# Optimization experiments

Measured on AMD Instinct MI355X. Metric: run time of the kernel, lower is better.

The kernel has to match this reference:

```python
import jax, jax.numpy as jnp
import numpy as np
import math

B_SZ, T_LEN, DIM = 1, 1024, 1024
D_STATE, EXPAND, NUM_SCALES, CONV_K = 16, 2, 3, 4
D_INNER = EXPAND * DIM
EPS_LOG = 1e-38
LN_EPS = 1e-5


def _causal_dwconv(x, w, b):
    # x: (B,T,D), w: (D,1,K) depthwise, b: (D,). torch Conv1d(pad=K-1)[:, :, :T] == left-pad K-1 (causal).
    y = jax.lax.conv_general_dilated(
        jnp.transpose(x, (0, 2, 1)), w, window_strides=(1,),
        padding=[(CONV_K - 1, 0)], dimension_numbers=('NCH', 'OIH', 'NCH'),
        feature_group_count=w.shape[0])
    return jnp.transpose(y, (0, 2, 1)) + b


def _ssm_core(x, cw, cb, xw, dtw, dtb, Dp):
    # x: (B,T,d_inner)
    xc = jax.nn.silu(_causal_dwconv(x, cw, cb))
    proj = xc @ xw.T                               # (B,T,2*d_state)
    B_ssm, C_ssm = proj[..., :D_STATE], proj[..., D_STATE:]
    dt = jax.nn.softplus(B_ssm @ dtw.T + dtb)      # (B,T,d_inner)
    dt = jax.nn.softplus(dt)                       # selective_scan applies softplus a second time (faithful)
    A = -jnp.arange(1, D_STATE + 1, dtype=xc.dtype)  # (d_state,) == -A_init row, same for every d_inner channel
    dA = jnp.exp(dt[..., None] * A)                # (B,T,d_inner,d_state)
    dBx = dt[..., None] * B_ssm[:, :, None, :] * xc[..., None]
    log_dA = jnp.log(jnp.clip(dA, EPS_LOG))
    log_dBx = jnp.log(jnp.clip(dBx, EPS_LOG))
    # parallel_scan_cpu: h = exp(cumsum(log_dA) + logcumsumexp(log_dBx - cumsum(log_dA)))
    a_star = jnp.cumsum(log_dA, axis=1)
    h = jnp.exp(a_star + jax.lax.cumlogsumexp(log_dBx - a_star, axis=1))
    return jnp.einsum('bts,btds->btd', C_ssm, h) + Dp * xc


def _downsample(x, stride):
    if stride == 1:
        return x
    Bb, T, D = x.shape
    Tt = (T // stride) * stride
    return x[:, :Tt].reshape(Bb, Tt // stride, stride, D).mean(2)


def _upsample(x, T_out):
    # F.interpolate(mode='linear', align_corners=False)
    T_in = x.shape[1]
    if T_in == T_out:
        return x
    scale = T_in / T_out
    pos = jnp.clip((jnp.arange(T_out, dtype=jnp.float32) + 0.5) * scale - 0.5, 0.0, T_in - 1)
    lo = jnp.floor(pos).astype(jnp.int32)
    hi = jnp.minimum(lo + 1, T_in - 1)
    w = (pos - lo.astype(pos.dtype))[None, :, None]
    return x[:, lo] * (1.0 - w) + x[:, hi] * w


def _forward(x, in_proj_w, conv_w, conv_b, xproj_w, dtproj_w, dtproj_b,
             D_param, scale_weights, gate_w1, gate_w2, out_proj_w, ln_g, ln_b):
    residual = x
    xz = x @ in_proj_w.T                           # (B,T,2*d_inner)
    x_in, gate = xz[..., :D_INNER], xz[..., D_INNER:]
    outs = []
    for s in range(NUM_SCALES):
        x_s = _downsample(x_in, 2 ** s)
        y_s = _ssm_core(x_s, conv_w[s], conv_b[s], xproj_w[s], dtproj_w[s], dtproj_b[s], D_param[s])
        outs.append(_upsample(y_s, x.shape[1]))
    w = jax.nn.softmax(scale_weights)
    fused = sum(w[s] * outs[s] for s in range(NUM_SCALES))
    ctx = sum(outs) / NUM_SCALES
    gate_ctx = jax.nn.sigmoid(jax.nn.silu(ctx @ gate_w1.T) @ gate_w2.T)
    out = (fused * gate_ctx) * jax.nn.silu(gate)
    out = out @ out_proj_w.T
    y = out + residual
    mu = y.mean(-1, keepdims=True)
    var = ((y - mu) ** 2).mean(-1, keepdims=True)
    return (y - mu) / jnp.sqrt(var + LN_EPS) * ln_g + ln_b


def setup_inputs() -> dict:
    key = jax.random.key(0)
    ks = jax.random.split(key, 12)
    g = lambda k, shp, s: (jax.random.normal(k, shp, jnp.float32) * s)
    return {
        'x': g(ks[0], (B_SZ, T_LEN, DIM), 1.0),
        'in_proj_w': g(ks[1], (2 * D_INNER, DIM), DIM ** -0.5),
        'conv_w': g(ks[2], (NUM_SCALES, D_INNER, 1, CONV_K), CONV_K ** -0.5),
        'conv_b': g(ks[3], (NUM_SCALES, D_INNER), 0.02),
        'xproj_w': g(ks[4], (NUM_SCALES, 2 * D_STATE, D_INNER), D_INNER ** -0.5),
        'dtproj_w': g(ks[5], (NUM_SCALES, D_INNER, D_STATE), D_STATE ** -0.5),
        'dtproj_b': jax.random.uniform(ks[6], (NUM_SCALES, D_INNER), jnp.float32,
                                       math.log(0.001), math.log(0.1)),
        'D_param': jnp.ones((NUM_SCALES, D_INNER), jnp.float32),
        'scale_weights': jnp.ones((NUM_SCALES,), jnp.float32) / NUM_SCALES,
        'gate_w1': g(ks[7], (D_INNER // 2, D_INNER), D_INNER ** -0.5),
        'gate_w2': g(ks[8], (D_INNER, D_INNER // 2), (D_INNER // 2) ** -0.5),
        'out_proj_w': g(ks[9], (DIM, D_INNER), D_INNER ** -0.5),
        'ln_g': jnp.ones((DIM,), jnp.float32),
        'ln_b': jnp.zeros((DIM,), jnp.float32),
    }


def reference(x, in_proj_w, conv_w, conv_b, xproj_w, dtproj_w, dtproj_b,
              D_param, scale_weights, gate_w1, gate_w2, out_proj_w, ln_g, ln_b):
    return _forward(x, in_proj_w, conv_w, conv_b, xproj_w, dtproj_w, dtproj_b,
                    D_param, scale_weights, gate_w1, gate_w2, out_proj_w, ln_g, ln_b)
```

## Files before the change

kernel.cpp:

```cpp
#include <hip/hip_runtime.h>

typedef unsigned short u16;
typedef float floatx4 __attribute__((ext_vector_type(4)));
typedef short shortx8 __attribute__((ext_vector_type(8)));

#define DIN 2048

__device__ __forceinline__ u16 f2bf(float f){
  unsigned u = __float_as_uint(f);
  u = (u + 0x7fffu + ((u>>16)&1u))>>16;
  return (u16)u;
}
__device__ __forceinline__ float sigf(float x){ return 1.f/(1.f+__expf(-x)); }
__device__ __forceinline__ float siluf(float x){ return x*sigf(x); }
__device__ __forceinline__ float softplusf(float x){ return fmaxf(x,0.f)+log1pf(__expf(-fabsf(x))); }

__device__ __forceinline__ void gld_lds16(const void* g, void* l){
  __builtin_amdgcn_global_load_lds((const __attribute__((address_space(1))) unsigned*)g,
                                   (__attribute__((address_space(3))) unsigned*)l, 16, 0, 0);
}

#define OFF_WINP  0ull
#define OFF_WG1   8388608ull
#define OFF_WG2   12582912ull
#define OFF_WOP   16777216ull
#define OFF_XB    20971520ull
#define OFF_XIN   23068672ull
#define OFF_SGATE 31457280ull
#define OFF_X1    39845888ull
#define OFF_X2    44040192ull
#define OFF_XC0   46137344ull
#define OFF_XC1   54525952ull
#define OFF_XC2   58720256ull
#define OFF_FUSED 60817408ull
#define OFF_G3O   69206016ull
#define OFF_Y0    75497472ull
#define OFF_Y1    83886080ull
#define OFF_Y2    88080384ull
#define OFF_P0    90177536ull
#define OFF_P1    90308608ull
#define OFF_P2    90374144ull
#define OFF_CTXB  OFF_XC0
#define OFF_T1B   OFF_XC1
#define OFF_PS    OFF_Y0
#define OFF_HINIT OFF_XIN
#define OFF_T1A0  OFF_XIN
#define OFF_T1A1  OFF_X1
#define OFF_YPA0  OFF_Y1
#define OFF_YPA1  (OFF_XC0 + 4194304ull)

__global__ __launch_bounds__(256) void cvt_kernel(
    const float* __restrict__ s0, u16* __restrict__ d0,
    const float* __restrict__ s1, u16* __restrict__ d1,
    const float* __restrict__ s2, u16* __restrict__ d2,
    const float* __restrict__ s3, u16* __restrict__ d3,
    const float* __restrict__ s4, u16* __restrict__ d4)
{
  int i = (blockIdx.x*256 + threadIdx.x)*4;
  const float* s; u16* d;
  if      (i <  4194304){ s=s0; d=d0; }
  else if (i <  6291456){ s=s1; d=d1; i -=  4194304; }
  else if (i <  8388608){ s=s2; d=d2; i -=  6291456; }
  else if (i < 10485760){ s=s3; d=d3; i -=  8388608; }
  else                  { s=s4; d=d4; i -= 10485760; }
  const float4 v = *(const float4*)(s + i);
  ushort4 o; o.x = f2bf(v.x); o.y = f2bf(v.y); o.z = f2bf(v.z); o.w = f2bf(v.w);
  *(ushort4*)(d + i) = o;
}

template<int MODE, int BM>
__global__ __launch_bounds__(256) void gemm_bt(
    const u16* __restrict__ A, const u16* __restrict__ B,
    int N, int K, int Ks,
    float* __restrict__ out_f, float* __restrict__ out_f2, u16* __restrict__ out_b,
    const float* __restrict__ ex0f, const float* __restrict__ ex1f,
    float* __restrict__ ex0, float* __restrict__ ex1)
{
  constexpr int NI = BM/32;
  constexpr int IP = BM/64;
  __shared__ u16 smA[2][BM*32];
  __shared__ u16 smB[2][BM*32];
  const int tid  = threadIdx.x;
  const int m0   = blockIdx.y * BM;
  const int n0   = blockIdx.x * BM;
  const int wv   = tid >> 6;
  const int lane = tid & 63;
  const int mw   = (wv >> 1) * (BM/2);
  const int nw   = (wv & 1) * (BM/2);
  const int quad = lane >> 4;
  const int l16  = lane & 15;
  const int srow = tid >> 2;
  const int scol = (tid & 3) * 8;

  floatx4 acc[NI][NI];
#pragma unroll
  for (int i=0;i<NI;i++)
#pragma unroll
    for (int j=0;j<NI;j++) acc[i][j] = (floatx4)0.f;

  const int kStart = blockIdx.z * Ks;
  const int kEnd   = kStart + Ks;

  auto stage = [&](int buf, int k0){
#pragma unroll
    for (int p=0;p<IP;p++){
      gld_lds16(A + (size_t)(m0 + p*64 + srow)*K + k0 + scol, &smA[buf][p*2048 + wv*512]);
      gld_lds16(B + (size_t)(n0 + p*64 + srow)*K + k0 + scol, &smB[buf][p*2048 + wv*512]);
    }
  };

  stage(0, kStart);
  int cur = 0;
  for (int k0 = kStart; k0 < kEnd; k0 += 32) {
    __syncthreads();
    if (k0 + 32 < kEnd) stage(cur^1, k0+32);
    shortx8 af[NI], bfr[NI];
#pragma unroll
    for (int i=0;i<NI;i++){
      af[i]  = *(const shortx8*)&smA[cur][(mw + i*16 + l16)*32 + quad*8];
      bfr[i] = *(const shortx8*)&smB[cur][(nw + i*16 + l16)*32 + quad*8];
    }
#pragma unroll
    for (int i=0;i<NI;i++)
#pragma unroll
      for (int j=0;j<NI;j++)
        acc[i][j] = __builtin_amdgcn_mfma_f32_16x16x32_bf16(af[i], bfr[j], acc[i][j], 0, 0, 0);
    cur ^= 1;
  }

#pragma unroll
  for (int i=0;i<NI;i++){
    const int mb = m0 + mw + i*16 + quad*4;
#pragma unroll
    for (int j=0;j<NI;j++){
      const int n = n0 + nw + j*16 + l16;
      const floatx4 v4 = acc[i][j];
      if (MODE == 0){
        if (n < 2048){
#pragma unroll
          for (int r=0;r<4;r++) out_f[(size_t)(mb+r)*2048 + n] = v4[r];
          ex0[(size_t)(mb>>1)*2048 + n]       = 0.5f*(v4[0]+v4[1]);
          ex0[(size_t)((mb>>1)+1)*2048 + n]   = 0.5f*(v4[2]+v4[3]);
          ex1[(size_t)(mb>>2)*2048 + n]       = 0.25f*(v4[0]+v4[1]+v4[2]+v4[3]);
        } else {
#pragma unroll
          for (int r=0;r<4;r++) out_f2[(size_t)(mb+r)*2048 + (n-2048)] = siluf(v4[r]);
        }
      } else if (MODE == 2){
#pragma unroll
        for (int r=0;r<4;r++){
          const size_t idx = (size_t)(mb+r)*N + n;
          out_b[idx] = f2bf(sigf(v4[r]) * ex0f[idx] * ex1f[idx]);
        }
      } else {
        float* dst = blockIdx.z ? out_f2 : out_f;
#pragma unroll
        for (int r=0;r<4;r++) dst[(size_t)(mb+r)*N + n] = v4[r];
      }
    }
  }
}

__global__ __launch_bounds__(256) void g2_epi(const float* __restrict__ a,
    const float* __restrict__ b, u16* __restrict__ o){
  const int i = (blockIdx.x*256 + threadIdx.x)*4;
  const float4 va = *(const float4*)(a+i);
  const float4 vb = *(const float4*)(b+i);
  ushort4 r;
  r.x = f2bf(siluf(va.x+vb.x)); r.y = f2bf(siluf(va.y+vb.y));
  r.z = f2bf(siluf(va.z+vb.z)); r.w = f2bf(siluf(va.w+vb.w));
  *(ushort4*)(o+i) = r;
}

__global__ __launch_bounds__(256) void conv_kernel(const float* __restrict__ xin,
    const float* __restrict__ x1, const float* __restrict__ x2,
    const float* __restrict__ cw, const float* __restrict__ cb,
    float* __restrict__ xc0, float* __restrict__ xc1, float* __restrict__ xc2){
  const int idx = blockIdx.x*256 + threadIdx.x;
  const float* xs; float* xc; int s, local;
  if (idx < 1024*DIN)              { s=0; local=idx;             xs=xin; xc=xc0; }
  else if (idx < (1024+512)*DIN)   { s=1; local=idx-1024*DIN;    xs=x1;  xc=xc1; }
  else                             { s=2; local=idx-1536*DIN;    xs=x2;  xc=xc2; }
  const int t = local >> 11, d = local & 2047;
  const float* w = cw + ((size_t)(s*DIN) + d)*4;
  float acc = cb[s*DIN + d];
#pragma unroll
  for (int j=0;j<4;j++){
    const int tt = t - 3 + j;
    if (tt >= 0) acc += w[j] * xs[(size_t)tt*DIN + d];
  }
  xc[local] = siluf(acc);
}

__global__ __launch_bounds__(256) void xproj_kernel(const float* __restrict__ xc0,
    const float* __restrict__ xc1, const float* __restrict__ xc2,
    const float* __restrict__ xw,
    float* __restrict__ p0, float* __restrict__ p1, float* __restrict__ p2){
  __shared__ float srow[DIN];
  const int b = blockIdx.x;
  const float* xc; float* proj; int s, t;
  if (b < 1024)      { s=0; t=b;       xc=xc0; proj=p0; }
  else if (b < 1536) { s=1; t=b-1024;  xc=xc1; proj=p1; }
  else               { s=2; t=b-1536;  xc=xc2; proj=p2; }
  const float* xr = xc + (size_t)t*DIN;
  const int tid = threadIdx.x;
#pragma unroll
  for (int q=0;q<2;q++){
    const int k = (q*256 + tid)*4;
    *(float4*)&srow[k] = *(const float4*)&xr[k];
  }
  __syncthreads();
  const int i = tid >> 3;
  const int j = tid & 7;
  const float* w = xw + ((size_t)s*32 + i)*DIN;
  float acc = 0.f;
#pragma unroll 8
  for (int c=0;c<256;c++){
    const int k = j + 8*c;
    acc += srow[k]*w[k];
  }
  acc += __shfl_xor(acc,1); acc += __shfl_xor(acc,2); acc += __shfl_xor(acc,4);
  if (j == 0) proj[t*32 + i] = acc;
}

__global__ __launch_bounds__(256) void scan_p1(
    const float* __restrict__ xc0, const float* __restrict__ xc1, const float* __restrict__ xc2,
    const float* __restrict__ p0,  const float* __restrict__ p1,  const float* __restrict__ p2,
    const float* __restrict__ dtw, const float* __restrict__ dtb,
    float2* __restrict__ PS)
{
  __shared__ float sproj[32*32];
  int b = blockIdx.x;
  const float *xc, *proj; int base, s;
  if (b < 256)      { xc=xc0; proj=p0; base=0;  s=0; }
  else if (b < 384) { b-=256; xc=xc1; proj=p1; base=32; s=1; }
  else              { b-=384; xc=xc2; proj=p2; base=48; s=2; }
  const int chunk = b >> 3;
  const int d     = (b & 7)*256 + threadIdx.x;
  const int t0    = chunk*32;
  {
    const int k = threadIdx.x*4;
    *(float4*)&sproj[k] = *(const float4*)&proj[t0*32 + k];
  }
  __syncthreads();

  float wreg[16];
  const float* wr = dtw + ((size_t)(s*DIN) + d)*16;
#pragma unroll
  for (int n=0;n<16;n++) wreg[n] = wr[n];
  const float bias = dtb[s*DIN + d];

  float H[16], P[16];
#pragma unroll
  for (int n=0;n<16;n++){ H[n]=0.f; P[n]=1.f; }
  const float* xcp = xc + (size_t)t0*DIN + d;
  float xcn = xcp[0];
  for (int tt=0; tt<32; tt++){
    const float xcv = xcn;
    if (tt < 31) xcn = xcp[(size_t)(tt+1)*DIN];
    const float* Bp = &sproj[tt*32];
    float bs = bias;
#pragma unroll
    for (int n=0;n<16;n++) bs += Bp[n]*wreg[n];
    const float dtv = softplusf(softplusf(bs));
    const float e = __expf(-dtv);
    const float c = dtv*xcv;
    float ep = e;
#pragma unroll
    for (int n=0;n<16;n++){
      const float dA  = fmaxf(ep, 1e-38f);
      const float dBx = fmaxf(c*Bp[n], 1e-38f);
      H[n] = dA*H[n] + dBx;
      P[n] *= dA;
      ep *= e;
    }
  }
  float2* o = PS + ((size_t)(base+chunk)*2048 + d)*16;
#pragma unroll
  for (int n=0;n<16;n++){ float2 v; v.x=P[n]; v.y=H[n]; o[n]=v; }
}

__global__ __launch_bounds__(256) void scan_combine(const float2* __restrict__ PS,
                                                    float* __restrict__ Hinit){
  int id = blockIdx.x*256 + threadIdx.x;
  int base, C;
  if (id < 32768)      { base=0;  C=32; }
  else if (id < 65536) { id-=32768; base=32; C=16; }
  else                 { id-=65536; base=48; C=8;  }
  const size_t off = (size_t)base*32768 + id;
  const float2* ps = PS + off;
  float* hi = Hinit + off;
  float H = 0.f;
  for (int c=0;c<C;c++){
    hi[(size_t)c*32768] = H;
    const float2 v = ps[(size_t)c*32768];
    H = v.x*H + v.y;
  }
}

__global__ __launch_bounds__(256) void scan_p2(
    const float* __restrict__ xc0, const float* __restrict__ xc1, const float* __restrict__ xc2,
    const float* __restrict__ p0,  const float* __restrict__ p1,  const float* __restrict__ p2,
    const float* __restrict__ dtw, const float* __restrict__ dtb,
    const float* __restrict__ Hinit, const float* __restrict__ Dp_all,
    float* __restrict__ y0, float* __restrict__ y1, float* __restrict__ y2)
{
  __shared__ float sproj[32*32];
  int b = blockIdx.x;
  const float *xc, *proj; float* y; int base, s;
  if (b < 256)      { xc=xc0; proj=p0; y=y0; base=0;  s=0; }
  else if (b < 384) { b-=256; xc=xc1; proj=p1; y=y1; base=32; s=1; }
  else              { b-=384; xc=xc2; proj=p2; y=y2; base=48; s=2; }
  const int chunk = b >> 3;
  const int d     = (b & 7)*256 + threadIdx.x;
  const int t0    = chunk*32;
  {
    const int k = threadIdx.x*4;
    *(float4*)&sproj[k] = *(const float4*)&proj[t0*32 + k];
  }
  __syncthreads();

  float wreg[16];
  const float* wr = dtw + ((size_t)(s*DIN) + d)*16;
#pragma unroll
  for (int n=0;n<16;n++) wreg[n] = wr[n];
  const float bias = dtb[s*DIN + d];

  float H[16];
  const float* hi = Hinit + ((size_t)(base+chunk)*2048 + d)*16;
#pragma unroll
  for (int n=0;n<16;n++) H[n] = hi[n];
  const float Dv = Dp_all[s*DIN + d];
  const float* xcp = xc + (size_t)t0*DIN + d;
  float* yp = y + (size_t)t0*DIN + d;
  float xcn = xcp[0];
  for (int tt=0; tt<32; tt++){
    const float xcv = xcn;
    if (tt < 31) xcn = xcp[(size_t)(tt+1)*DIN];
    const float* Bp = &sproj[tt*32];
    float bs = bias;
#pragma unroll
    for (int n=0;n<16;n++) bs += Bp[n]*wreg[n];
    const float dtv = softplusf(softplusf(bs));
    const float e = __expf(-dtv);
    const float c = dtv*xcv;
    float ep = e;
    float pacc = 0.f;
#pragma unroll
    for (int n=0;n<16;n++){
      const float dA  = fmaxf(ep, 1e-38f);
      const float dBx = fmaxf(c*Bp[n], 1e-38f);
      H[n] = dA*H[n] + dBx;
      pacc += Bp[16+n]*H[n];
      ep *= e;
    }
    yp[(size_t)tt*DIN] = pacc + Dv*xcv;
  }
}

__device__ __forceinline__ float ups_read(const float* __restrict__ ys, int Tin, int t, int d){
  const float scale = (float)Tin * (1.f/1024.f);
  float pos = ((float)t + 0.5f)*scale - 0.5f;
  pos = fminf(fmaxf(pos, 0.f), (float)(Tin-1));
  const int lo = (int)floorf(pos);
  const float w = pos - (float)lo;
  const int hi = min(lo+1, Tin-1);
  return ys[(size_t)lo*DIN + d]*(1.f-w) + ys[(size_t)hi*DIN + d]*w;
}

__global__ __launch_bounds__(256) void fuse_kernel(const float* __restrict__ y0,
    const float* __restrict__ y1, const float* __restrict__ y2,
    const float* __restrict__ sw, u16* __restrict__ ctxb, float* __restrict__ fused){
  const int idx = blockIdx.x*256 + threadIdx.x;
  const int t = idx >> 11, d = idx & 2047;
  const float w0r = sw[0], w1r = sw[1], w2r = sw[2];
  const float mx = fmaxf(w0r, fmaxf(w1r, w2r));
  float e0 = __expf(w0r-mx), e1 = __expf(w1r-mx), e2 = __expf(w2r-mx);
  const float inv = 1.f/(e0+e1+e2);
  e0 *= inv; e1 *= inv; e2 *= inv;
  const float o0 = y0[idx];
  const float o1 = ups_read(y1, 512, t, d);
  const float o2 = ups_read(y2, 256, t, d);
  fused[idx] = e0*o0 + e1*o1 + e2*o2;
  ctxb[idx]  = f2bf((o0+o1+o2)*(1.f/3.f));
}

__global__ __launch_bounds__(256) void ln_kernel(const float* __restrict__ ya,
    const float* __restrict__ yb, const float* __restrict__ xr,
    const float* __restrict__ g, const float* __restrict__ b, float* __restrict__ out){
  __shared__ float red[4];
  const int t = blockIdx.x;
  const size_t ro = (size_t)t*1024;
  float v[4];
  float s = 0.f;
#pragma unroll
  for (int i=0;i<4;i++){
    const int c = threadIdx.x + i*256;
    v[i] = ya[ro+c] + yb[ro+c] + xr[ro+c];
    s += v[i];
  }
  s += __shfl_xor(s,1); s += __shfl_xor(s,2); s += __shfl_xor(s,4);
  s += __shfl_xor(s,8); s += __shfl_xor(s,16); s += __shfl_xor(s,32);
  if ((threadIdx.x & 63) == 0) red[threadIdx.x>>6] = s;
  __syncthreads();
  const float mu = (red[0]+red[1]+red[2]+red[3]) * (1.f/1024.f);
  __syncthreads();
  float q = 0.f;
#pragma unroll
  for (int i=0;i<4;i++){ const float dd = v[i]-mu; q += dd*dd; }
  q += __shfl_xor(q,1); q += __shfl_xor(q,2); q += __shfl_xor(q,4);
  q += __shfl_xor(q,8); q += __shfl_xor(q,16); q += __shfl_xor(q,32);
  if ((threadIdx.x & 63) == 0) red[threadIdx.x>>6] = q;
  __syncthreads();
  const float rstd = rsqrtf((red[0]+red[1]+red[2]+red[3]) * (1.f/1024.f) + 1e-5f);
#pragma unroll
  for (int i=0;i<4;i++){
    const int c = threadIdx.x + i*256;
    out[ro + c] = (v[i]-mu)*rstd*g[c] + b[c];
  }
}

extern "C" void kernel_launch(void* const* d_in, const int* in_sizes, int n_in,
                              void* d_out, int out_size, void* d_ws, size_t ws_size,
                              hipStream_t stream) {
  const float* x     = (const float*)d_in[0];
  const float* inpw  = (const float*)d_in[1];
  const float* convw = (const float*)d_in[2];
  const float* convb = (const float*)d_in[3];
  const float* xpw   = (const float*)d_in[4];
  const float* dtw   = (const float*)d_in[5];
  const float* dtb   = (const float*)d_in[6];
  const float* Dp    = (const float*)d_in[7];
  const float* sw    = (const float*)d_in[8];
  const float* gw1   = (const float*)d_in[9];
  const float* gw2   = (const float*)d_in[10];
  const float* opw   = (const float*)d_in[11];
  const float* lng   = (const float*)d_in[12];
  const float* lnb   = (const float*)d_in[13];
  float* out = (float*)d_out;

  char* ws = (char*)d_ws;
  u16*    wInp  = (u16*)   (ws + OFF_WINP);
  u16*    wG1   = (u16*)   (ws + OFF_WG1);
  u16*    wG2   = (u16*)   (ws + OFF_WG2);
  u16*    wOp   = (u16*)   (ws + OFF_WOP);
  u16*    xb    = (u16*)   (ws + OFF_XB);
  float*  xin   = (float*) (ws + OFF_XIN);
  float*  sgate = (float*) (ws + OFF_SGATE);
  float*  x1    = (float*) (ws + OFF_X1);
  float*  x2    = (float*) (ws + OFF_X2);
  float*  xc0   = (float*) (ws + OFF_XC0);
  float*  xc1   = (float*) (ws + OFF_XC1);
  float*  xc2   = (float*) (ws + OFF_XC2);
  float*  y0    = (float*) (ws + OFF_Y0);
  float*  y1    = (float*) (ws + OFF_Y1);
  float*  y2    = (float*) (ws + OFF_Y2);
  float*  p0    = (float*) (ws + OFF_P0);
  float*  p1    = (float*) (ws + OFF_P1);
  float*  p2    = (float*) (ws + OFF_P2);
  float2* PS    = (float2*)(ws + OFF_PS);
  float*  Hinit = (float*) (ws + OFF_HINIT);
  u16*    ctxb  = (u16*)   (ws + OFF_CTXB);
  u16*    t1b   = (u16*)   (ws + OFF_T1B);
  float*  fused = (float*) (ws + OFF_FUSED);
  u16*    g3o   = (u16*)   (ws + OFF_G3O);
  float*  t1a0  = (float*) (ws + OFF_T1A0);
  float*  t1a1  = (float*) (ws + OFF_T1A1);
  float*  ypa0  = (float*) (ws + OFF_YPA0);
  float*  ypa1  = (float*) (ws + OFF_YPA1);

  cvt_kernel<<<11264, 256, 0, stream>>>(inpw, wInp, gw1, wG1, gw2, wG2, opw, wOp, x, xb);
  gemm_bt<0,64><<<dim3(64, 16, 1), 256, 0, stream>>>(xb, wInp, 4096, 1024, 1024,
                                                     xin, sgate, nullptr, nullptr, nullptr, x1, x2);
  conv_kernel<<<(1792*DIN)/256, 256, 0, stream>>>(xin, x1, x2, convw, convb, xc0, xc1, xc2);
  xproj_kernel<<<1792, 256, 0, stream>>>(xc0, xc1, xc2, xpw, p0, p1, p2);
  scan_p1<<<448, 256, 0, stream>>>(xc0, xc1, xc2, p0, p1, p2, dtw, dtb, PS);
  scan_combine<<<384, 256, 0, stream>>>(PS, Hinit);
  scan_p2<<<448, 256, 0, stream>>>(xc0, xc1, xc2, p0, p1, p2, dtw, dtb,
                                   Hinit, Dp, y0, y1, y2);
  fuse_kernel<<<(1024*DIN)/256, 256, 0, stream>>>(y0, y1, y2, sw, ctxb, fused);
  gemm_bt<4,64><<<dim3(16, 16, 2), 256, 0, stream>>>(ctxb, wG1, 1024, 2048, 1024,
                                                     t1a0, t1a1, nullptr, nullptr, nullptr, nullptr, nullptr);
  g2_epi<<<1024, 256, 0, stream>>>(t1a0, t1a1, t1b);
  gemm_bt<2,64><<<dim3(32, 16, 1), 256, 0, stream>>>(t1b, wG2, 2048, 1024, 1024,
                                                     nullptr, nullptr, g3o, fused, sgate, nullptr, nullptr);
  gemm_bt<4,64><<<dim3(16, 16, 2), 256, 0, stream>>>(g3o, wOp, 1024, 2048, 1024,
                                                     ypa0, ypa1, nullptr, nullptr, nullptr, nullptr, nullptr);
  ln_kernel<<<1024, 256, 0, stream>>>(ypa0, ypa1, x, lng, lnb, out);
}
```

Before: 343.8 us.

## Split scan state across thread pairs, cache dt, and use closed-form chunk decay

```diff
diff --git a/kernel.cpp b/kernel.cpp
--- a/kernel.cpp
+++ b/kernel.cpp
@@ -48,6 +48,9 @@
 #define OFF_T1A1  OFF_X1
 #define OFF_YPA0  OFF_Y1
 #define OFF_YPA1  (OFF_XC0 + 4194304ull)
+#define OFF_DT0   OFF_FUSED
+#define OFF_DT1   OFF_G3O
+#define OFF_DT2   (OFF_G3O + 4194304ull)
 
 __global__ __launch_bounds__(256) void cvt_kernel(
     const float* __restrict__ s0, u16* __restrict__ d0,
@@ -227,57 +230,64 @@
     const float* __restrict__ xc0, const float* __restrict__ xc1, const float* __restrict__ xc2,
     const float* __restrict__ p0,  const float* __restrict__ p1,  const float* __restrict__ p2,
     const float* __restrict__ dtw, const float* __restrict__ dtb,
+    float* __restrict__ dt0, float* __restrict__ dt1, float* __restrict__ dt2,
     float2* __restrict__ PS)
 {
   __shared__ float sproj[32*32];
   int b = blockIdx.x;
-  const float *xc, *proj; int base, s;
-  if (b < 256)      { xc=xc0; proj=p0; base=0;  s=0; }
-  else if (b < 384) { b-=256; xc=xc1; proj=p1; base=32; s=1; }
-  else              { b-=384; xc=xc2; proj=p2; base=48; s=2; }
-  const int chunk = b >> 3;
-  const int d     = (b & 7)*256 + threadIdx.x;
+  const float *xc, *proj; float* dto; int base, s;
+  if (b < 512)      { xc=xc0; proj=p0; dto=dt0; base=0;  s=0; }
+  else if (b < 768) { b-=512; xc=xc1; proj=p1; dto=dt1; base=32; s=1; }
+  else              { b-=768; xc=xc2; proj=p2; dto=dt2; base=48; s=2; }
+  const int chunk = b >> 4;
+  const int tid   = threadIdx.x;
+  const int d     = (b & 15)*128 + (tid >> 1);
+  const int half  = tid & 1;
+  const int n0    = half*8;
   const int t0    = chunk*32;
-  {
-    const int k = threadIdx.x*4;
-    *(float4*)&sproj[k] = *(const float4*)&proj[t0*32 + k];
-  }
-  __syncthreads();
-
-  float wreg[16];
-  const float* wr = dtw + ((size_t)(s*DIN) + d)*16;
-#pragma unroll
-  for (int n=0;n<16;n++) wreg[n] = wr[n];
+  { const int k = tid*4; *(float4*)&sproj[k] = *(const float4*)&proj[t0*32 + k]; }
+  __syncthreads();
+
+  float wreg[8];
+  const float* wr = dtw + ((size_t)(s*DIN) + d)*16 + n0;
+#pragma unroll
+  for (int k=0;k<8;k++) wreg[k] = wr[k];
   const float bias = dtb[s*DIN + d];
 
-  float H[16], P[16];
-#pragma unroll
-  for (int n=0;n<16;n++){ H[n]=0.f; P[n]=1.f; }
+  float H[8];
+#pragma unroll
+  for (int k=0;k<8;k++) H[k] = 0.f;
+  float S = 0.f;
   const float* xcp = xc + (size_t)t0*DIN + d;
-  float xcn = xcp[0];
+  float* dtp = dto + (size_t)t0*DIN + d;
   for (int tt=0; tt<32; tt++){
-    const float xcv = xcn;
-    if (tt < 31) xcn = xcp[(size_t)(tt+1)*DIN];
+    const float xcv = xcp[(size_t)tt*DIN];
     const float* Bp = &sproj[tt*32];
-    float bs = bias;
-#pragma unroll
-    for (int n=0;n<16;n++) bs += Bp[n]*wreg[n];
-    const float dtv = softplusf(softplusf(bs));
+    float bs = 0.f;
+#pragma unroll
+    for (int k=0;k<8;k++) bs += Bp[n0+k]*wreg[k];
+    bs += __shfl_xor(bs, 1);
+    const float dtv = softplusf(softplusf(bs + bias));
+    if (half == 0) dtp[(size_t)tt*DIN] = dtv;
+    S += dtv;
     const float e = __expf(-dtv);
+    const float e2 = e*e, e4 = e2*e2, e8 = e4*e4;
+    float ep = half ? e8*e : e;
     const float c = dtv*xcv;
-    float ep = e;
-#pragma unroll
-    for (int n=0;n<16;n++){
+#pragma unroll
+    for (int k=0;k<8;k++){
       const float dA  = fmaxf(ep, 1e-38f);
-      const float dBx = fmaxf(c*Bp[n], 1e-38f);
-      H[n] = dA*H[n] + dBx;
-      P[n] *= dA;
+      const float dBx = fmaxf(c*Bp[n0+k], 1e-38f);
+      H[k] = dA*H[k] + dBx;
       ep *= e;
     }
   }
-  float2* o = PS + ((size_t)(base+chunk)*2048 + d)*16;
-#pragma unroll
-  for (int n=0;n<16;n++){ float2 v; v.x=P[n]; v.y=H[n]; o[n]=v; }
+  const float q = __expf(-S);
+  const float q2 = q*q, q4 = q2*q2, q8 = q4*q4;
+  float qp = half ? q8*q : q;
+  float2* o = PS + ((size_t)(base+chunk)*2048 + d)*16 + n0;
+#pragma unroll
+  for (int k=0;k<8;k++){ float2 v; v.x = qp; v.y = H[k]; o[k] = v; qp *= q; }
 }
 
 __global__ __launch_bounds__(256) void scan_combine(const float2* __restrict__ PS,
@@ -301,60 +311,52 @@
 __global__ __launch_bounds__(256) void scan_p2(
     const float* __restrict__ xc0, const float* __restrict__ xc1, const float* __restrict__ xc2,
     const float* __restrict__ p0,  const float* __restrict__ p1,  const float* __restrict__ p2,
-    const float* __restrict__ dtw, const float* __restrict__ dtb,
+    const float* __restrict__ dt0, const float* __restrict__ dt1, const float* __restrict__ dt2,
     const float* __restrict__ Hinit, const float* __restrict__ Dp_all,
     float* __restrict__ y0, float* __restrict__ y1, float* __restrict__ y2)
 {
   __shared__ float sproj[32*32];
   int b = blockIdx.x;
-  const float *xc, *proj; float* y; int base, s;
-  if (b < 256)      { xc=xc0; proj=p0; y=y0; base=0;  s=0; }
-  else if (b < 384) { b-=256; xc=xc1; proj=p1; y=y1; base=32; s=1; }
-  else              { b-=384; xc=xc2; proj=p2; y=y2; base=48; s=2; }
-  const int chunk = b >> 3;
-  const int d     = (b & 7)*256 + threadIdx.x;
+  const float *xc, *proj, *dti; float* y; int base, s;
+  if (b < 512)      { xc=xc0; proj=p0; dti=dt0; y=y0; base=0;  s=0; }
+  else if (b < 768) { b-=512; xc=xc1; proj=p1; dti=dt1; y=y1; base=32; s=1; }
+  else              { b-=768; xc=xc2; proj=p2; dti=dt2; y=y2; base=48; s=2; }
+  const int chunk = b >> 4;
+  const int tid   = threadIdx.x;
+  const int d     = (b & 15)*128 + (tid >> 1);
+  const int half  = tid & 1;
+  const int n0    = half*8;
   const int t0    = chunk*32;
-  {
-    const int k = threadIdx.x*4;
-    *(float4*)&sproj[k] = *(const float4*)&proj[t0*32 + k];
-  }
-  __syncthreads();
-
-  float wreg[16];
-  const float* wr = dtw + ((size_t)(s*DIN) + d)*16;
-#pragma unroll
-  for (int n=0;n<16;n++) wreg[n] = wr[n];
-  const float bias = dtb[s*DIN + d];
-
-  float H[16];
-  const float* hi = Hinit + ((size_t)(base+chunk)*2048 + d)*16;
-#pragma unroll
-  for (int n=0;n<16;n++) H[n] = hi[n];
+  { const int k = tid*4; *(float4*)&sproj[k] = *(const float4*)&proj[t0*32 + k]; }
+  __syncthreads();
+
+  float H[8];
+  const float* hi = Hinit + ((size_t)(base+chunk)*2048 + d)*16 + n0;
+#pragma unroll
+  for (int k=0;k<8;k++) H[k] = hi[k];
   const float Dv = Dp_all[s*DIN + d];
   const float* xcp = xc + (size_t)t0*DIN + d;
+  const float* dtp = dti + (size_t)t0*DIN + d;
   float* yp = y + (size_t)t0*DIN + d;
-  float xcn = xcp[0];
   for (int tt=0; tt<32; tt++){
-    const float xcv = xcn;
-    if (tt < 31) xcn = xcp[(size_t)(tt+1)*DIN];
+    const float xcv = xcp[(size_t)tt*DIN];
+    const float dtv = dtp[(size_t)tt*DIN];
     const float* Bp = &sproj[tt*32];
-    float bs = bias;
-#pragma unroll
-    for (int n=0;n<16;n++) bs += Bp[n]*wreg[n];
-    const float dtv = softplusf(softplusf(bs));
     const float e = __expf(-dtv);
+    const float e2 = e*e, e4 = e2*e2, e8 = e4*e4;
+    float ep = half ? e8*e : e;
     const float c = dtv*xcv;
-    float ep = e;
     float pacc = 0.f;
 #pragma unroll
-    for (int n=0;n<16;n++){
+    for (int k=0;k<8;k++){
       const float dA  = fmaxf(ep, 1e-38f);
-      const float dBx = fmaxf(c*Bp[n], 1e-38f);
-      H[n] = dA*H[n] + dBx;
-      pacc += Bp[16+n]*H[n];
+      const float dBx = fmaxf(c*Bp[n0+k], 1e-38f);
+      H[k] = dA*H[k] + dBx;
+      pacc += Bp[16+n0+k]*H[k];
       ep *= e;
     }
-    yp[(size_t)tt*DIN] = pacc + Dv*xcv;
+    pacc += __shfl_xor(pacc, 1);
+    if (half == 0) yp[(size_t)tt*DIN] = pacc + Dv*xcv;
   }
 }
 
@@ -452,6 +454,9 @@
   float*  xc0   = (float*) (ws + OFF_XC0);
   float*  xc1   = (float*) (ws + OFF_XC1);
   float*  xc2   = (float*) (ws + OFF_XC2);
+  float*  dt0   = (float*) (ws + OFF_DT0);
+  float*  dt1   = (float*) (ws + OFF_DT1);
+  float*  dt2   = (float*) (ws + OFF_DT2);
   float*  y0    = (float*) (ws + OFF_Y0);
   float*  y1    = (float*) (ws + OFF_Y1);
   float*  y2    = (float*) (ws + OFF_Y2);
@@ -474,9 +479,10 @@
                                                      xin, sgate, nullptr, nullptr, nullptr, x1, x2);
   conv_kernel<<<(1792*DIN)/256, 256, 0, stream>>>(xin, x1, x2, convw, convb, xc0, xc1, xc2);
   xproj_kernel<<<1792, 256, 0, stream>>>(xc0, xc1, xc2, xpw, p0, p1, p2);
-  scan_p1<<<448, 256, 0, stream>>>(xc0, xc1, xc2, p0, p1, p2, dtw, dtb, PS);
+  scan_p1<<<896, 256, 0, stream>>>(xc0, xc1, xc2, p0, p1, p2, dtw, dtb,
+                                   dt0, dt1, dt2, PS);
   scan_combine<<<384, 256, 0, stream>>>(PS, Hinit);
-  scan_p2<<<448, 256, 0, stream>>>(xc0, xc1, xc2, p0, p1, p2, dtw, dtb,
+  scan_p2<<<896, 256, 0, stream>>>(xc0, xc1, xc2, p0, p1, p2, dt0, dt1, dt2,
                                    Hinit, Dp, y0, y1, y2);
   fuse_kernel<<<(1024*DIN)/256, 256, 0, stream>>>(y0, y1, y2, sw, ctxb, fused);
   gemm_bt<4,64><<<dim3(16, 16, 2), 256, 0, stream>>>(ctxb, wG1, 1024, 2048, 1024,
```

New measurement: 336.9 us. 2.0% less time.
